# Performance work log

Measured on AMD Instinct MI355X. Metric: run time of the kernel, lower is better.

## Reference

```python
import jax, jax.numpy as jnp
import numpy as np

B, C, H, W = 4, 256, 48, 48
NUM_HEADS = 8
HEAD_DIM = C // NUM_HEADS
LN_EPS = 1e-5


def setup_inputs() -> dict:
    key = jax.random.key(0)
    ks = jax.random.split(key, 12)
    s = 1.0 / np.sqrt(C)
    return {
        "x": jax.random.normal(ks[0], (B, C, H, W), dtype=jnp.float32),
        "context": jax.random.normal(ks[1], (B, C, H, W), dtype=jnp.float32),
        "Wq": jax.random.uniform(ks[2], (C, C), jnp.float32, -s, s),
        "bq": jax.random.uniform(ks[3], (C,), jnp.float32, -s, s),
        "Wk": jax.random.uniform(ks[4], (C, C), jnp.float32, -s, s),
        "bk": jax.random.uniform(ks[5], (C,), jnp.float32, -s, s),
        "Wv": jax.random.uniform(ks[6], (C, C), jnp.float32, -s, s),
        "bv": jax.random.uniform(ks[7], (C,), jnp.float32, -s, s),
        "Wo": jax.random.uniform(ks[8], (C, C), jnp.float32, -s, s),
        "bo": jax.random.uniform(ks[9], (C,), jnp.float32, -s, s),
        "ln_w": jnp.ones((C,), jnp.float32),
        "ln_b": jnp.zeros((C,), jnp.float32),
    }


def reference(x, context, Wq, bq, Wk, bk, Wv, bv, Wo, bo, ln_w, ln_b):
    b, c, h, w = x.shape
    S = h * w
    # [B, S, C] token layout (x.view(B,C,-1).permute(0,2,1))
    x_flat = x.reshape(b, c, S).transpose(0, 2, 1)
    ctx_flat = context.reshape(b, c, S).transpose(0, 2, 1)
    # QKV projections (torch Linear: y = x @ W.T + b)
    q = (x_flat @ Wq.T + bq).reshape(b, S, NUM_HEADS, HEAD_DIM).transpose(0, 2, 1, 3)
    k = (ctx_flat @ Wk.T + bk).reshape(b, S, NUM_HEADS, HEAD_DIM).transpose(0, 2, 1, 3)
    v = (ctx_flat @ Wv.T + bv).reshape(b, S, NUM_HEADS, HEAD_DIM).transpose(0, 2, 1, 3)
    # attention: [B, heads, S, S]
    scores = jnp.einsum("bhqd,bhkd->bhqk", q, k) / np.sqrt(HEAD_DIM)
    attn = jax.nn.softmax(scores, axis=-1)  # dropout is identity in eval mode
    attended = jnp.einsum("bhqk,bhkd->bhqd", attn, v)
    attended = attended.transpose(0, 2, 1, 3).reshape(b, S, c)
    out = attended @ Wo.T + bo
    # residual + layernorm over channel dim
    y = out + x_flat
    mu = jnp.mean(y, axis=-1, keepdims=True)
    var = jnp.var(y, axis=-1, keepdims=True)
    y = (y - mu) * jax.lax.rsqrt(var + LN_EPS) * ln_w + ln_b
    return y.transpose(0, 2, 1).reshape(b, c, h, w)
```

## Files before the change

### kernel.cpp

```cpp
#include <hip/hip_runtime.h>

#define B_ 4
#define C_ 256
#define S_ 2304
#define NH_ 8
#define HD_ 32
#define QS_L2E (0.17677669529663687f * 1.4426950408889634f)

typedef __attribute__((ext_vector_type(8))) __bf16 b16x8;
typedef __attribute__((ext_vector_type(4))) __bf16 b16x4;
typedef __attribute__((ext_vector_type(4))) float f32x4;
typedef __attribute__((ext_vector_type(4))) unsigned u32x4;

static __device__ __forceinline__ f32x4 mfma_bf16(b16x8 a, b16x8 b, f32x4 c) {
  return __builtin_amdgcn_mfma_f32_16x16x32_bf16(a, b, c, 0, 0, 0);
}

__global__ __launch_bounds__(256) void k_cvtw(
    const float* __restrict__ Wq, const float* __restrict__ Wk,
    const float* __restrict__ Wv, const float* __restrict__ Wo,
    __bf16* __restrict__ Wb, __bf16* __restrict__ Wob) {
  const int e = blockIdx.x * 1024 + threadIdx.x * 4;
  const float* s;
  __bf16* d;
  if (e < 196608) {
    const int m = e >> 16;
    s = (m == 0 ? Wq : (m == 1 ? Wk : Wv)) + (e & 65535);
    d = Wb + e;
  } else {
    s = Wo + (e - 196608);
    d = Wob + (e - 196608);
  }
  f32x4 v = *(const f32x4*)s;
  b16x4 o;
#pragma unroll
  for (int j = 0; j < 4; ++j) o[j] = (__bf16)v[j];
  *(b16x4*)d = o;
}

__global__ __launch_bounds__(256) void k_qkv(
    const float* __restrict__ x, const float* __restrict__ ctx,
    const __bf16* __restrict__ Wb,
    const float* __restrict__ bq, const float* __restrict__ bk, const float* __restrict__ bv,
    __bf16* __restrict__ Q, __bf16* __restrict__ Kd, __bf16* __restrict__ Vt) {
  __shared__ __bf16 lx[16][264];
  const int t = threadIdx.x;
  const int wid = t >> 6;
  const int lane = t & 63;
  const int col = lane & 15, g = lane >> 4;
  int r = blockIdx.x;
  const int p = r / 576; r %= 576;
  const int b = r / 144;
  const int s0 = (r % 144) * 16;
  const float* src = (p == 0 ? x : ctx) + (size_t)b * C_ * S_ + s0;
  const __bf16* W = Wb + p * 65536;
  const float* bias = p == 0 ? bq : (p == 1 ? bk : bv);
  const int i0 = wid * 64;
  const __bf16* arow = W + (size_t)(i0 + col) * C_ + g * 8;

  b16x8 af0 = *(const b16x8*)(arow);
  b16x8 af1 = *(const b16x8*)(arow + (size_t)16 * C_);
  b16x8 af2 = *(const b16x8*)(arow + (size_t)32 * C_);
  b16x8 af3 = *(const b16x8*)(arow + (size_t)48 * C_);

  {
    const int cr = t >> 2, sq = (t & 3) * 4;
#pragma unroll
    for (int j = 0; j < 4; ++j) {
      const int c = j * 64 + cr;
      f32x4 v = *(const f32x4*)(src + (size_t)c * S_ + sq);
#pragma unroll
      for (int jj = 0; jj < 4; ++jj) lx[sq + jj][c] = (__bf16)v[jj];
    }
  }
  __syncthreads();

  f32x4 acc[4] = {};
  b16x8 bf = *(const b16x8*)(&lx[col][g * 8]);

  for (int kk = 0; kk < 8; ++kk) {
    const int nk = ((kk + 1) & 7) * 32;
    b16x8 nbf = *(const b16x8*)(&lx[col][nk + g * 8]);
    b16x8 naf0 = *(const b16x8*)(arow + nk);
    b16x8 naf1 = *(const b16x8*)(arow + (size_t)16 * C_ + nk);
    b16x8 naf2 = *(const b16x8*)(arow + (size_t)32 * C_ + nk);
    b16x8 naf3 = *(const b16x8*)(arow + (size_t)48 * C_ + nk);
    __builtin_amdgcn_sched_barrier(0);
    acc[0] = mfma_bf16(af0, bf, acc[0]);
    acc[1] = mfma_bf16(af1, bf, acc[1]);
    acc[2] = mfma_bf16(af2, bf, acc[2]);
    acc[3] = mfma_bf16(af3, bf, acc[3]);
    bf = nbf; af0 = naf0; af1 = naf1; af2 = naf2; af3 = naf3;
  }
  const int tok = s0 + col;
#pragma unroll
  for (int j = 0; j < 4; ++j) {
    const int ib = i0 + j * 16 + g * 4;
    f32x4 bi = *(const f32x4*)(bias + ib);
    const int h = ib >> 5, d0 = ib & 31;
    const size_t bh = (size_t)b * NH_ + h;
    if (p == 2) {
#pragma unroll
      for (int rr = 0; rr < 4; ++rr)
        Vt[(bh * HD_ + d0 + rr) * S_ + tok] = (__bf16)(acc[j][rr] + bi[rr]);
    } else if (p == 1) {
      b16x4 o;
#pragma unroll
      for (int rr = 0; rr < 4; ++rr) o[rr] = (__bf16)(acc[j][rr] + bi[rr]);
      *(b16x4*)(Kd + (bh * S_ + tok) * HD_ + d0) = o;
    } else {
      b16x4 o;
#pragma unroll
      for (int rr = 0; rr < 4; ++rr) o[rr] = (__bf16)((acc[j][rr] + bi[rr]) * QS_L2E);
      *(b16x4*)(Q + (bh * S_ + tok) * HD_ + d0) = o;
    }
  }
}

__global__ __launch_bounds__(256) void k_attn(
    const __bf16* __restrict__ Q, const __bf16* __restrict__ Kd,
    const __bf16* __restrict__ Vt, __bf16* __restrict__ att) {
  __shared__ float mrg[3][2][656];
  int bid = blockIdx.x;
  bid = (bid & 7) * 288 + (bid >> 3);
  const int wid = threadIdx.x >> 6;
  const int lane = threadIdx.x & 63;
  const int col = lane & 15, g = lane >> 4;
  const int bh = bid / 72;
  const int s0 = (bid % 72) * 32;
  const int b = bh >> 3, h = bh & 7;
  const __bf16* Qb = Q + (size_t)bh * S_ * HD_;
  const __bf16* Kb = Kd + (size_t)bh * S_ * HD_;
  const __bf16* Vb = Vt + (size_t)bh * HD_ * S_;

  b16x8 qfr[2];
#pragma unroll
  for (int q = 0; q < 2; ++q)
    qfr[q] = *(const b16x8*)(Qb + (size_t)(s0 + q * 16 + col) * HD_ + g * 8);
  const int kA = ((col >> 2) * 8) + (col & 3);
  const int kbeg = wid * (S_ / 4);

  b16x8 onesf;
#pragma unroll
  for (int j = 0; j < 8; ++j) onesf[j] = (__bf16)1.0f;

  f32x4 acc0[2] = {}, acc1[2] = {}, accl[2] = {};
  const f32x4 zero = {};

  const __bf16* kptr = Kb + (size_t)(kbeg + kA) * HD_ + g * 8;
  const __bf16* vptr = Vb + (size_t)col * S_ + kbeg + g * 8;

  b16x8 ka = *(const b16x8*)(kptr);
  b16x8 kb = *(const b16x8*)(kptr + 4 * HD_);
  b16x8 v0 = *(const b16x8*)(vptr);
  b16x8 v1 = *(const b16x8*)(vptr + 16 * S_);

  for (int it = 0; it < S_ / 4 / 32; ++it) {
    kptr += 32 * HD_; vptr += 32;
    b16x8 ka_n = *(const b16x8*)(kptr);
    b16x8 kb_n = *(const b16x8*)(kptr + 4 * HD_);
    b16x8 v0_n = *(const b16x8*)(vptr);
    b16x8 v1_n = *(const b16x8*)(vptr + 16 * S_);
    __builtin_amdgcn_sched_barrier(0);

#pragma unroll
    for (int q = 0; q < 2; ++q) {
      f32x4 sA = mfma_bf16(ka, qfr[q], zero);
      f32x4 sB = mfma_bf16(kb, qfr[q], zero);
      float eA0 = __builtin_amdgcn_exp2f(sA[0]);
      float eA1 = __builtin_amdgcn_exp2f(sA[1]);
      float eA2 = __builtin_amdgcn_exp2f(sA[2]);
      float eA3 = __builtin_amdgcn_exp2f(sA[3]);
      float eB0 = __builtin_amdgcn_exp2f(sB[0]);
      float eB1 = __builtin_amdgcn_exp2f(sB[1]);
      float eB2 = __builtin_amdgcn_exp2f(sB[2]);
      float eB3 = __builtin_amdgcn_exp2f(sB[3]);
      unsigned w0, w1, w2, w3;
      asm("v_cvt_pk_bf16_f32 %0, %1, %2" : "=v"(w0) : "v"(eA0), "v"(eA1));
      asm("v_cvt_pk_bf16_f32 %0, %1, %2" : "=v"(w1) : "v"(eA2), "v"(eA3));
      asm("v_cvt_pk_bf16_f32 %0, %1, %2" : "=v"(w2) : "v"(eB0), "v"(eB1));
      asm("v_cvt_pk_bf16_f32 %0, %1, %2" : "=v"(w3) : "v"(eB2), "v"(eB3));
      u32x4 pw = {w0, w1, w2, w3};
      b16x8 pf = __builtin_bit_cast(b16x8, pw);
      acc0[q] = mfma_bf16(pf, v0, acc0[q]);
      acc1[q] = mfma_bf16(pf, v1, acc1[q]);
      accl[q] = mfma_bf16(pf, onesf, accl[q]);
    }
    ka = ka_n; kb = kb_n; v0 = v0_n; v1 = v1_n;
  }

  if (wid > 0) {
#pragma unroll
    for (int qt = 0; qt < 2; ++qt) {
      float* m0 = mrg[wid - 1][qt];
      *(f32x4*)(m0 + col * 20 + g * 4) = acc0[qt];
      *(f32x4*)(m0 + 320 + col * 20 + g * 4) = acc1[qt];
      if (col == 0) *(f32x4*)(m0 + 640 + g * 4) = accl[qt];
    }
  }
  __syncthreads();
  if (wid == 0) {
#pragma unroll
    for (int qt = 0; qt < 2; ++qt) {
      f32x4 t0 = acc0[qt], t1 = acc1[qt], tl = accl[qt];
#pragma unroll
      for (int m = 0; m < 3; ++m) {
        const float* pm = mrg[m][qt];
        t0 += *(const f32x4*)(pm + col * 20 + g * 4);
        t1 += *(const f32x4*)(pm + 320 + col * 20 + g * 4);
        tl += *(const f32x4*)(pm + 640 + g * 4);
      }
#pragma unroll
      for (int j = 0; j < 4; ++j) {
        const int q = g * 4 + j;
        const float inv = 1.f / tl[j];
        const size_t obase = ((size_t)b * S_ + s0 + qt * 16 + q) * C_ + h * HD_;
        att[obase + col] = (__bf16)(t0[j] * inv);
        att[obase + 16 + col] = (__bf16)(t1[j] * inv);
      }
    }
  }
}

__global__ __launch_bounds__(256) void k_oln(
    const __bf16* __restrict__ att, const __bf16* __restrict__ Wob,
    const float* __restrict__ bo, const float* __restrict__ x,
    const float* __restrict__ lnw, const float* __restrict__ lnb,
    float* __restrict__ out) {
  __shared__ float part[4][2][16];
  __shared__ float lw[256], lb[256];
  const int wid = threadIdx.x >> 6;
  const int lane = threadIdx.x & 63;
  const int col = lane & 15, g = lane >> 4;
  int r = blockIdx.x;
  const int b = r / 144;
  const int s0 = (r % 144) * 16;
  const int i0 = wid * 64;
  lw[threadIdx.x] = lnw[threadIdx.x];
  lb[threadIdx.x] = lnb[threadIdx.x];

  f32x4 acc[4] = {};
  const __bf16* arow = att + ((size_t)b * S_ + s0 + col) * C_ + g * 8;
  const __bf16* wrow = Wob + (size_t)(i0 + col) * C_ + g * 8;

  b16x8 bfr = *(const b16x8*)(arow);
  b16x8 af0 = *(const b16x8*)(wrow);
  b16x8 af1 = *(const b16x8*)(wrow + (size_t)16 * C_);
  b16x8 af2 = *(const b16x8*)(wrow + (size_t)32 * C_);
  b16x8 af3 = *(const b16x8*)(wrow + (size_t)48 * C_);

  for (int kk = 0; kk < 8; ++kk) {
    const int nk = ((kk + 1) & 7) * 32;
    b16x8 nbfr = *(const b16x8*)(arow + nk);
    b16x8 naf0 = *(const b16x8*)(wrow + nk);
    b16x8 naf1 = *(const b16x8*)(wrow + (size_t)16 * C_ + nk);
    b16x8 naf2 = *(const b16x8*)(wrow + (size_t)32 * C_ + nk);
    b16x8 naf3 = *(const b16x8*)(wrow + (size_t)48 * C_ + nk);
    __builtin_amdgcn_sched_barrier(0);
    acc[0] = mfma_bf16(af0, bfr, acc[0]);
    acc[1] = mfma_bf16(af1, bfr, acc[1]);
    acc[2] = mfma_bf16(af2, bfr, acc[2]);
    acc[3] = mfma_bf16(af3, bfr, acc[3]);
    bfr = nbfr; af0 = naf0; af1 = naf1; af2 = naf2; af3 = naf3;
  }
  float s = 0.f, s2 = 0.f;
#pragma unroll
  for (int j = 0; j < 4; ++j) {
#pragma unroll
    for (int rr = 0; rr < 4; ++rr) {
      const int i = i0 + j * 16 + g * 4 + rr;
      float v = acc[j][rr] + bo[i] + x[((size_t)b * C_ + i) * S_ + s0 + col];
      acc[j][rr] = v;
      s += v; s2 += v * v;
    }
  }
  s += __shfl_xor(s, 16); s2 += __shfl_xor(s2, 16);
  s += __shfl_xor(s, 32); s2 += __shfl_xor(s2, 32);
  if (g == 0) { part[wid][0][col] = s; part[wid][1][col] = s2; }
  __syncthreads();
  float st = part[0][0][col] + part[1][0][col] + part[2][0][col] + part[3][0][col];
  float st2 = part[0][1][col] + part[1][1][col] + part[2][1][col] + part[3][1][col];
  const float mu = st * (1.f / 256.f);
  const float rs = rsqrtf(st2 * (1.f / 256.f) - mu * mu + 1e-5f);
#pragma unroll
  for (int j = 0; j < 4; ++j) {
#pragma unroll
    for (int rr = 0; rr < 4; ++rr) {
      const int i = i0 + j * 16 + g * 4 + rr;
      out[((size_t)b * C_ + i) * S_ + s0 + col] = (acc[j][rr] - mu) * rs * lw[i] + lb[i];
    }
  }
}

extern "C" void kernel_launch(void* const* d_in, const int* in_sizes, int n_in,
                              void* d_out, int out_size, void* d_ws, size_t ws_size,
                              hipStream_t stream) {
  const float* x   = (const float*)d_in[0];
  const float* ctx = (const float*)d_in[1];
  const float* Wq  = (const float*)d_in[2];
  const float* bq  = (const float*)d_in[3];
  const float* Wk  = (const float*)d_in[4];
  const float* bk  = (const float*)d_in[5];
  const float* Wv  = (const float*)d_in[6];
  const float* bv  = (const float*)d_in[7];
  const float* Wo  = (const float*)d_in[8];
  const float* bo  = (const float*)d_in[9];
  const float* lnw = (const float*)d_in[10];
  const float* lnb = (const float*)d_in[11];
  float* out = (float*)d_out;

  char* ws = (char*)d_ws;
  __bf16* Wb  = (__bf16*)(ws + 9437184);
  __bf16* Wob = (__bf16*)(ws + 9830400);
  __bf16* Kd  = (__bf16*)(ws + 9961472);
  __bf16* Vt  = (__bf16*)(ws + 14680064);
  __bf16* att = (__bf16*)(ws + 19398656);
  __bf16* Q   = (__bf16*)(ws + 24117248);

  k_cvtw <<< 256, 256, 0, stream>>>(Wq, Wk, Wv, Wo, Wb, Wob);
  k_qkv  <<<1728, 256, 0, stream>>>(x, ctx, Wb, bq, bk, bv, Q, Kd, Vt);
  k_attn <<<2304, 256, 0, stream>>>(Q, Kd, Vt, att);
  k_oln  <<< 576, 256, 0, stream>>>(att, Wob, bo, x, lnw, lnb, out);
}
```

Measured before the change: 195.9 us.

## Fuse weight bf16 conversion into GEMMs and double attention query tile

Removes the separate weight-conversion kernel. The QKV and output-projection GEMMs now load fp32 weights directly and convert them to bf16 in registers before each MFMA, which saves one launch and the round trip of the converted weights through memory. The attention kernel now processes 64 queries per block instead of 32, halving the grid. This reuses each loaded K/V fragment across four query tiles rather than two, at the cost of more registers, a larger shared merge buffer, and fewer blocks to fill the GPU.

After: 211.6 us. 8.0% more time.

```diff
diff --git a/kernel.cpp b/kernel.cpp
--- a/kernel.cpp
+++ b/kernel.cpp
@@ -16,31 +16,16 @@
   return __builtin_amdgcn_mfma_f32_16x16x32_bf16(a, b, c, 0, 0, 0);
 }
 
-__global__ __launch_bounds__(256) void k_cvtw(
-    const float* __restrict__ Wq, const float* __restrict__ Wk,
-    const float* __restrict__ Wv, const float* __restrict__ Wo,
-    __bf16* __restrict__ Wb, __bf16* __restrict__ Wob) {
-  const int e = blockIdx.x * 1024 + threadIdx.x * 4;
-  const float* s;
-  __bf16* d;
-  if (e < 196608) {
-    const int m = e >> 16;
-    s = (m == 0 ? Wq : (m == 1 ? Wk : Wv)) + (e & 65535);
-    d = Wb + e;
-  } else {
-    s = Wo + (e - 196608);
-    d = Wob + (e - 196608);
-  }
-  f32x4 v = *(const f32x4*)s;
-  b16x4 o;
-#pragma unroll
-  for (int j = 0; j < 4; ++j) o[j] = (__bf16)v[j];
-  *(b16x4*)d = o;
+static __device__ __forceinline__ b16x8 cvt_frag(f32x4 lo, f32x4 hi) {
+  b16x8 o;
+#pragma unroll
+  for (int i = 0; i < 4; ++i) { o[i] = (__bf16)lo[i]; o[4 + i] = (__bf16)hi[i]; }
+  return o;
 }
 
 __global__ __launch_bounds__(256) void k_qkv(
     const float* __restrict__ x, const float* __restrict__ ctx,
-    const __bf16* __restrict__ Wb,
+    const float* __restrict__ Wq, const float* __restrict__ Wk, const float* __restrict__ Wv,
     const float* __restrict__ bq, const float* __restrict__ bk, const float* __restrict__ bv,
     __bf16* __restrict__ Q, __bf16* __restrict__ Kd, __bf16* __restrict__ Vt) {
   __shared__ __bf16 lx[16][264];
@@ -53,15 +38,19 @@
   const int b = r / 144;
   const int s0 = (r % 144) * 16;
   const float* src = (p == 0 ? x : ctx) + (size_t)b * C_ * S_ + s0;
-  const __bf16* W = Wb + p * 65536;
+  const float* W = p == 0 ? Wq : (p == 1 ? Wk : Wv);
   const float* bias = p == 0 ? bq : (p == 1 ? bk : bv);
   const int i0 = wid * 64;
-  const __bf16* arow = W + (size_t)(i0 + col) * C_ + g * 8;
-
-  b16x8 af0 = *(const b16x8*)(arow);
-  b16x8 af1 = *(const b16x8*)(arow + (size_t)16 * C_);
-  b16x8 af2 = *(const b16x8*)(arow + (size_t)32 * C_);
-  b16x8 af3 = *(const b16x8*)(arow + (size_t)48 * C_);
+  const float* wrow = W + (size_t)(i0 + col) * C_ + g * 8;
+
+  f32x4 wlo0 = *(const f32x4*)(wrow);
+  f32x4 whi0 = *(const f32x4*)(wrow + 4);
+  f32x4 wlo1 = *(const f32x4*)(wrow + (size_t)16 * C_);
+  f32x4 whi1 = *(const f32x4*)(wrow + (size_t)16 * C_ + 4);
+  f32x4 wlo2 = *(const f32x4*)(wrow + (size_t)32 * C_);
+  f32x4 whi2 = *(const f32x4*)(wrow + (size_t)32 * C_ + 4);
+  f32x4 wlo3 = *(const f32x4*)(wrow + (size_t)48 * C_);
+  f32x4 whi3 = *(const f32x4*)(wrow + (size_t)48 * C_ + 4);
 
   {
     const int cr = t >> 2, sq = (t & 3) * 4;
@@ -81,16 +70,22 @@
   for (int kk = 0; kk < 8; ++kk) {
     const int nk = ((kk + 1) & 7) * 32;
     b16x8 nbf = *(const b16x8*)(&lx[col][nk + g * 8]);
-    b16x8 naf0 = *(const b16x8*)(arow + nk);
-    b16x8 naf1 = *(const b16x8*)(arow + (size_t)16 * C_ + nk);
-    b16x8 naf2 = *(const b16x8*)(arow + (size_t)32 * C_ + nk);
-    b16x8 naf3 = *(const b16x8*)(arow + (size_t)48 * C_ + nk);
+    f32x4 nlo0 = *(const f32x4*)(wrow + nk);
+    f32x4 nhi0 = *(const f32x4*)(wrow + nk + 4);
+    f32x4 nlo1 = *(const f32x4*)(wrow + (size_t)16 * C_ + nk);
+    f32x4 nhi1 = *(const f32x4*)(wrow + (size_t)16 * C_ + nk + 4);
+    f32x4 nlo2 = *(const f32x4*)(wrow + (size_t)32 * C_ + nk);
+    f32x4 nhi2 = *(const f32x4*)(wrow + (size_t)32 * C_ + nk + 4);
+    f32x4 nlo3 = *(const f32x4*)(wrow + (size_t)48 * C_ + nk);
+    f32x4 nhi3 = *(const f32x4*)(wrow + (size_t)48 * C_ + nk + 4);
     __builtin_amdgcn_sched_barrier(0);
-    acc[0] = mfma_bf16(af0, bf, acc[0]);
-    acc[1] = mfma_bf16(af1, bf, acc[1]);
-    acc[2] = mfma_bf16(af2, bf, acc[2]);
-    acc[3] = mfma_bf16(af3, bf, acc[3]);
-    bf = nbf; af0 = naf0; af1 = naf1; af2 = naf2; af3 = naf3;
+    acc[0] = mfma_bf16(cvt_frag(wlo0, whi0), bf, acc[0]);
+    acc[1] = mfma_bf16(cvt_frag(wlo1, whi1), bf, acc[1]);
+    acc[2] = mfma_bf16(cvt_frag(wlo2, whi2), bf, acc[2]);
+    acc[3] = mfma_bf16(cvt_frag(wlo3, whi3), bf, acc[3]);
+    bf = nbf;
+    wlo0 = nlo0; whi0 = nhi0; wlo1 = nlo1; whi1 = nhi1;
+    wlo2 = nlo2; whi2 = nhi2; wlo3 = nlo3; whi3 = nhi3;
   }
   const int tok = s0 + col;
 #pragma unroll
@@ -120,22 +115,22 @@
 __global__ __launch_bounds__(256) void k_attn(
     const __bf16* __restrict__ Q, const __bf16* __restrict__ Kd,
     const __bf16* __restrict__ Vt, __bf16* __restrict__ att) {
-  __shared__ float mrg[3][2][656];
+  __shared__ float mrg[3][4][656];
   int bid = blockIdx.x;
-  bid = (bid & 7) * 288 + (bid >> 3);
+  bid = (bid & 7) * 144 + (bid >> 3);
   const int wid = threadIdx.x >> 6;
   const int lane = threadIdx.x & 63;
   const int col = lane & 15, g = lane >> 4;
-  const int bh = bid / 72;
-  const int s0 = (bid % 72) * 32;
+  const int bh = bid / 36;
+  const int s0 = (bid % 36) * 64;
   const int b = bh >> 3, h = bh & 7;
   const __bf16* Qb = Q + (size_t)bh * S_ * HD_;
   const __bf16* Kb = Kd + (size_t)bh * S_ * HD_;
   const __bf16* Vb = Vt + (size_t)bh * HD_ * S_;
 
-  b16x8 qfr[2];
-#pragma unroll
-  for (int q = 0; q < 2; ++q)
+  b16x8 qfr[4];
+#pragma unroll
+  for (int q = 0; q < 4; ++q)
     qfr[q] = *(const b16x8*)(Qb + (size_t)(s0 + q * 16 + col) * HD_ + g * 8);
   const int kA = ((col >> 2) * 8) + (col & 3);
   const int kbeg = wid * (S_ / 4);
@@ -144,7 +139,7 @@
 #pragma unroll
   for (int j = 0; j < 8; ++j) onesf[j] = (__bf16)1.0f;
 
-  f32x4 acc0[2] = {}, acc1[2] = {}, accl[2] = {};
+  f32x4 acc0[4] = {}, acc1[4] = {}, accl[4] = {};
   const f32x4 zero = {};
 
   const __bf16* kptr = Kb + (size_t)(kbeg + kA) * HD_ + g * 8;
@@ -164,7 +159,7 @@
     __builtin_amdgcn_sched_barrier(0);
 
 #pragma unroll
-    for (int q = 0; q < 2; ++q) {
+    for (int q = 0; q < 4; ++q) {
       f32x4 sA = mfma_bf16(ka, qfr[q], zero);
       f32x4 sB = mfma_bf16(kb, qfr[q], zero);
       float eA0 = __builtin_amdgcn_exp2f(sA[0]);
@@ -191,7 +186,7 @@
 
   if (wid > 0) {
 #pragma unroll
-    for (int qt = 0; qt < 2; ++qt) {
+    for (int qt = 0; qt < 4; ++qt) {
       float* m0 = mrg[wid - 1][qt];
       *(f32x4*)(m0 + col * 20 + g * 4) = acc0[qt];
       *(f32x4*)(m0 + 320 + col * 20 + g * 4) = acc1[qt];
@@ -201,7 +196,7 @@
   __syncthreads();
   if (wid == 0) {
 #pragma unroll
-    for (int qt = 0; qt < 2; ++qt) {
+    for (int qt = 0; qt < 4; ++qt) {
       f32x4 t0 = acc0[qt], t1 = acc1[qt], tl = accl[qt];
 #pragma unroll
       for (int m = 0; m < 3; ++m) {
@@ -223,7 +218,7 @@
 }
 
 __global__ __launch_bounds__(256) void k_oln(
-    const __bf16* __restrict__ att, const __bf16* __restrict__ Wob,
+    const __bf16* __restrict__ att, const float* __restrict__ Wo,
     const float* __restrict__ bo, const float* __restrict__ x,
     const float* __restrict__ lnw, const float* __restrict__ lnb,
     float* __restrict__ out) {
@@ -241,27 +236,37 @@
 
   f32x4 acc[4] = {};
   const __bf16* arow = att + ((size_t)b * S_ + s0 + col) * C_ + g * 8;
-  const __bf16* wrow = Wob + (size_t)(i0 + col) * C_ + g * 8;
+  const float* wrow = Wo + (size_t)(i0 + col) * C_ + g * 8;
 
   b16x8 bfr = *(const b16x8*)(arow);
-  b16x8 af0 = *(const b16x8*)(wrow);
-  b16x8 af1 = *(const b16x8*)(wrow + (size_t)16 * C_);
-  b16x8 af2 = *(const b16x8*)(wrow + (size_t)32 * C_);
-  b16x8 af3 = *(const b16x8*)(wrow + (size_t)48 * C_);
+  f32x4 wlo0 = *(const f32x4*)(wrow);
+  f32x4 whi0 = *(const f32x4*)(wrow + 4);
+  f32x4 wlo1 = *(const f32x4*)(wrow + (size_t)16 * C_);
+  f32x4 whi1 = *(const f32x4*)(wrow + (size_t)16 * C_ + 4);
+  f32x4 wlo2 = *(const f32x4*)(wrow + (size_t)32 * C_);
+  f32x4 whi2 = *(const f32x4*)(wrow + (size_t)32 * C_ + 4);
+  f32x4 wlo3 = *(const f32x4*)(wrow + (size_t)48 * C_);
+  f32x4 whi3 = *(const f32x4*)(wrow + (size_t)48 * C_ + 4);
 
   for (int kk = 0; kk < 8; ++kk) {
     const int nk = ((kk + 1) & 7) * 32;
     b16x8 nbfr = *(const b16x8*)(arow + nk);
-    b16x8 naf0 = *(const b16x8*)(wrow + nk);
-    b16x8 naf1 = *(const b16x8*)(wrow + (size_t)16 * C_ + nk);
-    b16x8 naf2 = *(const b16x8*)(wrow + (size_t)32 * C_ + nk);
-    b16x8 naf3 = *(const b16x8*)(wrow + (size_t)48 * C_ + nk);
+    f32x4 nlo0 = *(const f32x4*)(wrow + nk);
+    f32x4 nhi0 = *(const f32x4*)(wrow + nk + 4);
+    f32x4 nlo1 = *(const f32x4*)(wrow + (size_t)16 * C_ + nk);
+    f32x4 nhi1 = *(const f32x4*)(wrow + (size_t)16 * C_ + nk + 4);
+    f32x4 nlo2 = *(const f32x4*)(wrow + (size_t)32 * C_ + nk);
+    f32x4 nhi2 = *(const f32x4*)(wrow + (size_t)32 * C_ + nk + 4);
+    f32x4 nlo3 = *(const f32x4*)(wrow + (size_t)48 * C_ + nk);
+    f32x4 nhi3 = *(const f32x4*)(wrow + (size_t)48 * C_ + nk + 4);
     __builtin_amdgcn_sched_barrier(0);
-    acc[0] = mfma_bf16(af0, bfr, acc[0]);
-    acc[1] = mfma_bf16(af1, bfr, acc[1]);
-    acc[2] = mfma_bf16(af2, bfr, acc[2]);
-    acc[3] = mfma_bf16(af3, bfr, acc[3]);
-    bfr = nbfr; af0 = naf0; af1 = naf1; af2 = naf2; af3 = naf3;
+    acc[0] = mfma_bf16(cvt_frag(wlo0, whi0), bfr, acc[0]);
+    acc[1] = mfma_bf16(cvt_frag(wlo1, whi1), bfr, acc[1]);
+    acc[2] = mfma_bf16(cvt_frag(wlo2, whi2), bfr, acc[2]);
+    acc[3] = mfma_bf16(cvt_frag(wlo3, whi3), bfr, acc[3]);
+    bfr = nbfr;
+    wlo0 = nlo0; whi0 = nhi0; wlo1 = nlo1; whi1 = nhi1;
+    wlo2 = nlo2; whi2 = nhi2; wlo3 = nlo3; whi3 = nhi3;
   }
   float s = 0.f, s2 = 0.f;
 #pragma unroll
@@ -310,15 +315,12 @@
   float* out = (float*)d_out;
 
   char* ws = (char*)d_ws;
-  __bf16* Wb  = (__bf16*)(ws + 9437184);
-  __bf16* Wob = (__bf16*)(ws + 9830400);
-  __bf16* Kd  = (__bf16*)(ws + 9961472);
-  __bf16* Vt  = (__bf16*)(ws + 14680064);
-  __bf16* att = (__bf16*)(ws + 19398656);
-  __bf16* Q   = (__bf16*)(ws + 24117248);
-
-  k_cvtw <<< 256, 256, 0, stream>>>(Wq, Wk, Wv, Wo, Wb, Wob);
-  k_qkv  <<<1728, 256, 0, stream>>>(x, ctx, Wb, bq, bk, bv, Q, Kd, Vt);
-  k_attn <<<2304, 256, 0, stream>>>(Q, Kd, Vt, att);
-  k_oln  <<< 576, 256, 0, stream>>>(att, Wob, bo, x, lnw, lnb, out);
-}
+  __bf16* Kd  = (__bf16*)(ws);
+  __bf16* Vt  = (__bf16*)(ws + 4718592);
+  __bf16* att = (__bf16*)(ws + 9437184);
+  __bf16* Q   = (__bf16*)(ws + 14155776);
+
+  k_qkv  <<<1728, 256, 0, stream>>>(x, ctx, Wq, Wk, Wv, bq, bk, bv, Q, Kd, Vt);
+  k_attn <<<1152, 256, 0, stream>>>(Q, Kd, Vt, att);
+  k_oln  <<< 576, 256, 0, stream>>>(att, Wo, bo, x, lnw, lnb, out);
+}
```
